# Performance work log

Hardware: AMD Instinct MI355X
Metric: run time of the kernel (lower is better)

## Reference

```python
import jax, jax.numpy as jnp
import numpy as np

N_EXPERTS = 16
TOP_K = 2
D_MODEL = 1024
D_FF = 1024
D_FF_SHARED = 2048
T_TOKENS = 4096


def setup_inputs() -> dict:
    key = jax.random.key(0)
    ks = jax.random.split(key, 7)
    s = 0.02
    return {
        "hidden_states": jax.random.normal(ks[0], (T_TOKENS, D_MODEL), jnp.float32),
        "gate_weight": jax.random.normal(ks[1], (N_EXPERTS, D_MODEL), jnp.float32) * s,
        "expert_gate_up": jax.random.normal(ks[2], (N_EXPERTS, 2 * D_FF, D_MODEL), jnp.float32) * s,
        "expert_down": jax.random.normal(ks[3], (N_EXPERTS, D_MODEL, D_FF), jnp.float32) * s,
        "shared_gate_up": jax.random.normal(ks[4], (2 * D_FF_SHARED, D_MODEL), jnp.float32) * s,
        "shared_down": jax.random.normal(ks[5], (D_MODEL, D_FF_SHARED), jnp.float32) * s,
        "shared_expert_gate_weight": jax.random.normal(ks[6], (1, D_MODEL), jnp.float32) * s,
    }


def _moe_forward(x, gate_weight, expert_gate_up, expert_down):
    T = x.shape[0]
    E = gate_weight.shape[0]
    # Router: top-k over logits, softmax over the selected logits (fp32)
    router_logits = x @ gate_weight.T                      # [T, E]
    topk_logits, topk_ids = jax.lax.top_k(router_logits, TOP_K)
    topk_weights = jax.nn.softmax(topk_logits.astype(jnp.float32), axis=-1)
    # Dense combine matrix C[t, e] = routing weight of expert e for token t
    combine = jnp.zeros((T, E), jnp.float32).at[
        jnp.arange(T)[:, None], topk_ids
    ].add(topk_weights)                                    # [T, E]

    # Scan over experts to avoid materializing [E, T, d]
    def body(acc, inputs):
        w_gu, w_d, c_e = inputs                            # [2F,d], [d,F], [T]
        gu = x @ w_gu.T                                    # [T, 2F]
        g, u = gu[:, :D_FF], gu[:, D_FF:]
        h = jax.nn.silu(g) * u                             # [T, F]
        acc = acc + c_e[:, None] * (h @ w_d.T)             # [T, d]
        return acc, None

    acc0 = jnp.zeros_like(x)
    moe_out, _ = jax.lax.scan(body, acc0, (expert_gate_up, expert_down, combine.T))
    return moe_out


def _shared_expert(x, shared_gate_up, shared_down, shared_expert_gate_weight):
    gu = x @ shared_gate_up.T                              # [T, 2Fs]
    mid = gu.shape[-1] // 2
    h = jax.nn.silu(gu[:, :mid]) * gu[:, mid:]
    out = h @ shared_down.T                                # [T, d]
    gate = jax.nn.sigmoid(x @ shared_expert_gate_weight.T)  # [T, 1]
    return out * gate


def reference(hidden_states, gate_weight, expert_gate_up, expert_down,
              shared_gate_up, shared_down, shared_expert_gate_weight):
    moe_out = _moe_forward(hidden_states, gate_weight, expert_gate_up, expert_down)
    shared_out = _shared_expert(hidden_states, shared_gate_up, shared_down,
                                shared_expert_gate_weight)
    return moe_out + shared_out
```

## Files before the change

kernel.cpp:

```cpp
#include <hip/hip_runtime.h>
#include <hip/hip_bf16.h>

#define T_TOKENS 4096
#define D_MODEL  1024
#define N_EXP    16
#define D_FF     1024
#define D_FF_SH  2048
#define MAX_T256 48

typedef __attribute__((ext_vector_type(8))) short short8;
typedef __attribute__((ext_vector_type(4))) float float4v;

__device__ __forceinline__ short f2bf(float f) {
    union { float f; unsigned u; } c; c.f = f;
    unsigned u = c.u + 0x7fffu + ((c.u >> 16) & 1u);
    return (short)(u >> 16);
}

__device__ __forceinline__ void gload16(const void* g, void* l) {
    __builtin_amdgcn_global_load_lds(
        (const __attribute__((address_space(1))) void*)g,
        (__attribute__((address_space(3))) void*)l, 16, 0, 0);
}

#define RING_TOP(VM) do { \
    asm volatile("s_waitcnt vmcnt(" #VM ") lgkmcnt(0)" ::: "memory"); \
    __builtin_amdgcn_s_barrier(); \
} while (0)

#define PHASE_BAR() do { \
    asm volatile("s_barrier" ::: "memory"); \
    __builtin_amdgcn_sched_barrier(0); \
} while (0)

__global__ __launch_bounds__(256) void convert_all_kernel(
    const float* __restrict__ s0, short* __restrict__ d0,
    const float* __restrict__ s1, short* __restrict__ d1,
    const float* __restrict__ s2, short* __restrict__ d2,
    const float* __restrict__ s3, short* __restrict__ d3) {
    int c = blockIdx.x * 256 + threadIdx.x;
    const float* s; short* d; int off;
    if      (c < 4194304) { s = s0; d = d0; off = c; }
    else if (c < 6291456) { s = s1; d = d1; off = c - 4194304; }
    else if (c < 6815744) { s = s2; d = d2; off = c - 6291456; }
    else                  { s = s3; d = d3; off = c - 6815744; }
    size_t i = (size_t)off * 8;
    float4 a = *(const float4*)(s + i);
    float4 b = *(const float4*)(s + i + 4);
    union { short sh[8]; int4 v; } p;
    p.sh[0] = f2bf(a.x); p.sh[1] = f2bf(a.y); p.sh[2] = f2bf(a.z); p.sh[3] = f2bf(a.w);
    p.sh[4] = f2bf(b.x); p.sh[5] = f2bf(b.y); p.sh[6] = f2bf(b.z); p.sh[7] = f2bf(b.w);
    *(int4*)(d + i) = p.v;
}

__global__ __launch_bounds__(256) void router_kernel(
    const float* __restrict__ x, const float* __restrict__ gw, const float* __restrict__ sgw,
    short* __restrict__ xb, int* __restrict__ topk_id, float* __restrict__ topk_w,
    float* __restrict__ gate, int* __restrict__ counts) {
    __shared__ float gwl[17 * 1024];
    int tid = threadIdx.x;
#pragma unroll
    for (int i = 0; i < 16; i++)
        *(float4*)&gwl[tid * 4 + i * 1024] = *(const float4*)&gw[tid * 4 + i * 1024];
    *(float4*)&gwl[16384 + tid * 4] = *(const float4*)&sgw[tid * 4];
    __syncthreads();

    int wave = tid >> 6, lane = tid & 63;
    int t0 = blockIdx.x * 16 + wave * 4;

    float acc[4][17];
#pragma unroll
    for (int tt = 0; tt < 4; tt++)
#pragma unroll
        for (int e = 0; e < 17; e++) acc[tt][e] = 0.f;

#pragma unroll
    for (int i = 0; i < 4; i++) {
        int d = lane * 4 + i * 256;
        float4 xv[4];
#pragma unroll
        for (int tt = 0; tt < 4; tt++) {
            xv[tt] = *(const float4*)&x[(size_t)(t0 + tt) * D_MODEL + d];
            union { short sh[4]; int2 v; } p;
            p.sh[0] = f2bf(xv[tt].x); p.sh[1] = f2bf(xv[tt].y);
            p.sh[2] = f2bf(xv[tt].z); p.sh[3] = f2bf(xv[tt].w);
            *(int2*)&xb[(size_t)(t0 + tt) * D_MODEL + d] = p.v;
        }
#pragma unroll
        for (int e = 0; e < 17; e++) {
            float4 g = *(const float4*)&gwl[e * 1024 + d];
#pragma unroll
            for (int tt = 0; tt < 4; tt++)
                acc[tt][e] += xv[tt].x * g.x + xv[tt].y * g.y + xv[tt].z * g.z + xv[tt].w * g.w;
        }
    }

#pragma unroll
    for (int tt = 0; tt < 4; tt++)
#pragma unroll
        for (int e = 0; e < 17; e++)
            for (int off = 32; off; off >>= 1) acc[tt][e] += __shfl_xor(acc[tt][e], off);

    if (lane == 0) {
#pragma unroll
        for (int tt = 0; tt < 4; tt++) {
            int t = t0 + tt;
            float v1 = -1e30f, v2 = -1e30f; int i1 = 0, i2 = 0;
#pragma unroll
            for (int e = 0; e < 16; e++) {
                float v = acc[tt][e];
                if (v > v1) { v2 = v1; i2 = i1; v1 = v; i1 = e; }
                else if (v > v2) { v2 = v; i2 = e; }
            }
            float e2 = expf(v2 - v1);
            float s = 1.f + e2;
            topk_id[t * 2] = i1; topk_id[t * 2 + 1] = i2;
            topk_w[t * 2] = 1.f / s; topk_w[t * 2 + 1] = e2 / s;
            gate[t] = 1.f / (1.f + expf(-acc[tt][16]));
            atomicAdd(&counts[i1], 1); atomicAdd(&counts[i2], 1);
        }
    }
}

__global__ void offsets_kernel(const int* __restrict__ counts, int* __restrict__ offsets,
                               int* __restrict__ cursor, int* __restrict__ tile_map,
                               int* __restrict__ n_tiles) {
    if (threadIdx.x == 0) {
        int off = 0, nt = 0;
        for (int e = 0; e < N_EXP; e++) {
            offsets[e] = off; cursor[e] = off;
            int c = counts[e];
            for (int r = 0; r < c; r += 256) tile_map[nt++] = (e << 16) | (r >> 8);
            off += c;
        }
        n_tiles[0] = nt;
    }
}

__global__ __launch_bounds__(256) void scatter_kernel(
    const int* __restrict__ topk_id, const float* __restrict__ topk_w,
    int* __restrict__ cursor, int* __restrict__ tok_list, float* __restrict__ tok_w,
    int* __restrict__ slot_of) {
    int t = blockIdx.x * 256 + threadIdx.x;
#pragma unroll
    for (int k = 0; k < 2; k++) {
        int e = topk_id[t * 2 + k];
        int pos = atomicAdd(&cursor[e], 1);
        tok_list[pos] = t;
        tok_w[pos] = topk_w[t * 2 + k];
        slot_of[t * 2 + k] = pos;
    }
}

__global__ __launch_bounds__(512, 2) void gemm1_kernel(
    const short* __restrict__ xb,
    const short* __restrict__ Wexp,
    const short* __restrict__ Wsh,
    short* __restrict__ Hexp,
    short* __restrict__ Hsh,
    const int* __restrict__ tok_list,
    const int* __restrict__ offsets, const int* __restrict__ counts,
    const int* __restrict__ tile_map, const int* __restrict__ n_tiles) {
    int bx = blockIdx.x, by = blockIdx.y;
    int count, row0, dff, col0;
    const int* idx = nullptr;
    const short* Wg; short* Hout;
    if (bx < MAX_T256) {
        if (bx >= n_tiles[0]) return;
        int tm = tile_map[bx];
        int e = tm >> 16; row0 = (tm & 0xffff) << 8;
        count = counts[e];
        int base = offsets[e];
        idx = tok_list + base;
        Wg = Wexp + (size_t)e * 2 * D_FF * D_MODEL;
        Hout = Hexp + (size_t)base * D_FF;
        dff = D_FF;
        col0 = by * 128;
    } else {
        int id = (bx - MAX_T256) * 8 + by;
        row0 = (id >> 4) * 256; count = T_TOKENS;
        Wg = Wsh; Hout = Hsh; dff = D_FF_SH;
        col0 = (id & 15) * 128;
    }
    const short* Wu = Wg + (size_t)dff * D_MODEL;

    __shared__ char lds[131072];

    int t = threadIdx.x;
    int wave = t >> 6, lane = t & 63;
    int wm = (wave & 3) * 64, wn = (wave >> 2) * 64;
    int fr = lane & 15;
    int fk2p = ((((lane >> 4) + (fr >> 1)) & 3) << 4);
    int rA = t >> 2;
    int csrc = ((t & 3) - (t >> 3)) & 3;
    int cq = csrc * 8;
    int lo = t * 16;

    int r0c = min(row0 + rA, count - 1);
    int r1c = min(row0 + rA + 128, count - 1);
    int g0 = idx ? idx[r0c] : r0c;
    int g1 = idx ? idx[r1c] : r1c;
    const short* aP0 = xb + (size_t)g0 * D_MODEL + cq;
    const short* aP1 = xb + (size_t)g1 * D_MODEL + cq;
    const short* bgP = Wg + (size_t)(col0 + rA) * D_MODEL + cq;
    const short* buP = Wu + (size_t)(col0 + rA) * D_MODEL + cq;

    float4v accg[4][4], accu[4][4];
#pragma unroll
    for (int i = 0; i < 4; i++)
#pragma unroll
        for (int j = 0; j < 4; j++) { accg[i][j] = (float4v)0.f; accu[i][j] = (float4v)0.f; }

    auto stage = [&](int s) {
        char* base = lds + (s & 3) * 32768;
        int off = s * 32;
        gload16(aP0 + off, base + lo);
        gload16(aP1 + off, base + 8192 + lo);
        gload16(bgP + off, base + 16384 + lo);
        gload16(buP + off, base + 24576 + lo);
    };

    auto step = [&](int k, bool pf) {
        const char* sb = lds + (k & 3) * 32768;
        char* nb = lds + ((k + 3) & 3) * 32768;
        int off3 = (k + 3) * 32;
        if (pf) { gload16(aP0 + off3, nb + lo); gload16(aP1 + off3, nb + 8192 + lo); }
        short8 af[4], bgf[4];
#pragma unroll
        for (int i = 0; i < 4; i++)
            af[i] = *(const short8*)(sb + (wm + i * 16 + fr) * 64 + fk2p);
#pragma unroll
        for (int j = 0; j < 4; j++)
            bgf[j] = *(const short8*)(sb + 16384 + (wn + j * 16 + fr) * 64 + fk2p);
        PHASE_BAR();
        __builtin_amdgcn_s_setprio(1);
#pragma unroll
        for (int i = 0; i < 4; i++)
#pragma unroll
            for (int j = 0; j < 4; j++)
                accg[i][j] = __builtin_amdgcn_mfma_f32_16x16x32_bf16(af[i], bgf[j], accg[i][j], 0, 0, 0);
        __builtin_amdgcn_s_setprio(0);
        if (pf) { gload16(bgP + off3, nb + 16384 + lo); gload16(buP + off3, nb + 24576 + lo); }
        short8 buf4[4];
#pragma unroll
        for (int j = 0; j < 4; j++)
            buf4[j] = *(const short8*)(sb + 24576 + (wn + j * 16 + fr) * 64 + fk2p);
        PHASE_BAR();
        __builtin_amdgcn_s_setprio(1);
#pragma unroll
        for (int i = 0; i < 4; i++)
#pragma unroll
            for (int j = 0; j < 4; j++)
                accu[i][j] = __builtin_amdgcn_mfma_f32_16x16x32_bf16(af[i], buf4[j], accu[i][j], 0, 0, 0);
        __builtin_amdgcn_s_setprio(0);
    };

    const int NK = D_MODEL / 32;
    stage(0); stage(1); stage(2);
    int k = 0;
    for (; k < NK - 3; ++k) { RING_TOP(8); step(k, true); }
    RING_TOP(8); step(k, false); ++k;
    RING_TOP(4); step(k, false); ++k;
    RING_TOP(0); step(k, false);

    int erow = (lane >> 4) * 4;
    int ecol = lane & 15;
#pragma unroll
    for (int i = 0; i < 4; i++)
#pragma unroll
        for (int j = 0; j < 4; j++)
#pragma unroll
            for (int r = 0; r < 4; r++) {
                int row = wm + i * 16 + erow + r;
                if (row0 + row < count) {
                    float g = accg[i][j][r], u = accu[i][j][r];
                    float h = g / (1.f + expf(-g)) * u;
                    Hout[(size_t)(row0 + row) * dff + col0 + wn + j * 16 + ecol] = f2bf(h);
                }
            }
}

__global__ __launch_bounds__(512, 4) void gemm2_kernel(
    const short* __restrict__ Hexp, const short* __restrict__ Hsh,
    const short* __restrict__ Wdexp,
    const short* __restrict__ Wdsh,
    float* __restrict__ oslots,
    float* __restrict__ out,
    const float* __restrict__ tok_w, const float* __restrict__ gate,
    const int* __restrict__ offsets, const int* __restrict__ counts,
    const int* __restrict__ tile_map, const int* __restrict__ n_tiles) {
    int bx = blockIdx.x, by = blockIdx.y;
    int count, row0, K, base, col0;
    const short* Ab; const short* B;
    bool shared_part;
    if (bx < 16) {
        int id = bx * 8 + by;
        row0 = (id >> 3) * 256; count = T_TOKENS; base = 0;
        Ab = Hsh; K = D_FF_SH; B = Wdsh; shared_part = true;
        col0 = (id & 7) * 128;
    } else {
        int q = bx - 16;
        if (q >= n_tiles[0]) return;
        int tm = tile_map[q];
        int e = tm >> 16; row0 = (tm & 0xffff) << 8;
        count = counts[e]; base = offsets[e];
        Ab = Hexp + (size_t)base * D_FF; K = D_FF;
        B = Wdexp + (size_t)e * D_MODEL * D_FF;
        shared_part = false;
        col0 = by * 128;
    }

    __shared__ char lds[73728];

    int t = threadIdx.x;
    int wave = t >> 6, lane = t & 63;
    int wm = (wave & 3) * 64, wn = (wave >> 2) * 64;
    int fr = lane & 15;
    int fk2p = ((((lane >> 4) + (fr >> 1)) & 3) << 4);
    int rA = t >> 2;
    int csrc = ((t & 3) - (t >> 3)) & 3;
    int cq = csrc * 8;
    int lo = t * 16;

    int r0c = min(row0 + rA, count - 1);
    int r1c = min(row0 + rA + 128, count - 1);
    const short* aP0 = Ab + (size_t)r0c * K + cq;
    const short* aP1 = Ab + (size_t)r1c * K + cq;
    const short* bP  = B + (size_t)(col0 + rA) * K + cq;

    float4v acc[4][4];
#pragma unroll
    for (int i = 0; i < 4; i++)
#pragma unroll
        for (int j = 0; j < 4; j++) acc[i][j] = (float4v)0.f;

    auto stage = [&](int pos, int s) {
        char* bb = lds + pos * 24576;
        int off = s * 32;
        gload16(aP0 + off, bb + lo);
        gload16(aP1 + off, bb + 8192 + lo);
        gload16(bP + off,  bb + 16384 + lo);
    };
    auto compute = [&](int pos) {
        const char* sb = lds + pos * 24576;
        short8 af[4], bf[4];
#pragma unroll
        for (int i = 0; i < 4; i++)
            af[i] = *(const short8*)(sb + (wm + i * 16 + fr) * 64 + fk2p);
#pragma unroll
        for (int j = 0; j < 4; j++)
            bf[j] = *(const short8*)(sb + 16384 + (wn + j * 16 + fr) * 64 + fk2p);
        __builtin_amdgcn_s_setprio(1);
#pragma unroll
        for (int i = 0; i < 4; i++)
#pragma unroll
            for (int j = 0; j < 4; j++)
                acc[i][j] = __builtin_amdgcn_mfma_f32_16x16x32_bf16(af[i], bf[j], acc[i][j], 0, 0, 0);
        __builtin_amdgcn_s_setprio(0);
    };

    const int NK = K / 32;
    stage(0, 0); stage(1, 1);
    int k = 0, spos = 2, cpos = 0;
    for (; k < NK - 2; ++k) {
        RING_TOP(3);
        stage(spos, k + 2); spos = (spos == 2) ? 0 : spos + 1;
        compute(cpos);      cpos = (cpos == 2) ? 0 : cpos + 1;
    }
    RING_TOP(3); compute(cpos); cpos = (cpos == 2) ? 0 : cpos + 1; ++k;
    RING_TOP(0); compute(cpos);

    int erow = (lane >> 4) * 4;
    int ecol = lane & 15;
#pragma unroll
    for (int i = 0; i < 4; i++)
#pragma unroll
        for (int j = 0; j < 4; j++)
#pragma unroll
            for (int r = 0; r < 4; r++) {
                int row = wm + i * 16 + erow + r;
                if (row0 + row < count) {
                    float v = acc[i][j][r];
                    int col = col0 + wn + j * 16 + ecol;
                    if (!shared_part) {
                        int slot = base + row0 + row;
                        oslots[(size_t)slot * D_MODEL + col] = tok_w[slot] * v;
                    } else {
                        out[(size_t)(row0 + row) * D_MODEL + col] = gate[row0 + row] * v;
                    }
                }
            }
}

__global__ __launch_bounds__(256) void combine_kernel(
    float* __restrict__ out, const float* __restrict__ oslots,
    const int* __restrict__ slot_of) {
    int t = blockIdx.x;
    int sA = slot_of[t * 2], sB = slot_of[t * 2 + 1];
    int d = threadIdx.x * 4;
    float4 o = *(float4*)&out[(size_t)t * D_MODEL + d];
    float4 a = *(const float4*)&oslots[(size_t)sA * D_MODEL + d];
    float4 b = *(const float4*)&oslots[(size_t)sB * D_MODEL + d];
    o.x += a.x + b.x; o.y += a.y + b.y; o.z += a.z + b.z; o.w += a.w + b.w;
    *(float4*)&out[(size_t)t * D_MODEL + d] = o;
}

extern "C" void kernel_launch(void* const* d_in, const int* in_sizes, int n_in,
                              void* d_out, int out_size, void* d_ws, size_t ws_size,
                              hipStream_t stream) {
    const float* x     = (const float*)d_in[0];
    const float* gw    = (const float*)d_in[1];
    const float* egu   = (const float*)d_in[2];
    const float* edown = (const float*)d_in[3];
    const float* sgu   = (const float*)d_in[4];
    const float* sdown = (const float*)d_in[5];
    const float* sgate = (const float*)d_in[6];
    float* out = (float*)d_out;
    char* ws = (char*)d_ws;

    const size_t XB_OFF     = 0;
    const size_t WGU_OFF    = XB_OFF     + (size_t)4096*1024*2;
    const size_t WDOWN_OFF  = WGU_OFF    + (size_t)16*2048*1024*2;
    const size_t WSGU_OFF   = WDOWN_OFF  + (size_t)16*1024*1024*2;
    const size_t WSDOWN_OFF = WSGU_OFF   + (size_t)4096*1024*2;
    const size_t HEXP_OFF   = WSDOWN_OFF + (size_t)1024*2048*2;
    const size_t HSH_OFF    = HEXP_OFF   + (size_t)8192*1024*2;
    const size_t OSLOT_OFF  = HSH_OFF    + (size_t)4096*2048*2;
    const size_t TID_OFF    = OSLOT_OFF  + (size_t)8192*1024*4;
    const size_t TW_OFF     = TID_OFF    + 4096*2*4;
    const size_t GATE_OFF   = TW_OFF     + 4096*2*4;
    const size_t TOKL_OFF   = GATE_OFF   + 4096*4;
    const size_t TOKW_OFF   = TOKL_OFF   + 8192*4;
    const size_t SLOT_OFF   = TOKW_OFF   + 8192*4;
    const size_t CNT_OFF    = SLOT_OFF   + 8192*4;
    const size_t OFFS_OFF   = CNT_OFF    + 256;
    const size_t CUR_OFF    = OFFS_OFF   + 256;
    const size_t TMAP_OFF   = CUR_OFF    + 256;
    const size_t NT_OFF     = TMAP_OFF   + 512;

    short* xb      = (short*)(ws + XB_OFF);
    short* wgu_b   = (short*)(ws + WGU_OFF);
    short* wdown_b = (short*)(ws + WDOWN_OFF);
    short* wsgu_b  = (short*)(ws + WSGU_OFF);
    short* wsdn_b  = (short*)(ws + WSDOWN_OFF);
    short* h_exp   = (short*)(ws + HEXP_OFF);
    short* h_sh    = (short*)(ws + HSH_OFF);
    float* oslots  = (float*)(ws + OSLOT_OFF);
    int*   topk_id = (int*)(ws + TID_OFF);
    float* topk_w  = (float*)(ws + TW_OFF);
    float* gate    = (float*)(ws + GATE_OFF);
    int*   tok_l   = (int*)(ws + TOKL_OFF);
    float* tok_w   = (float*)(ws + TOKW_OFF);
    int*   slot_of = (int*)(ws + SLOT_OFF);
    int*   counts  = (int*)(ws + CNT_OFF);
    int*   offsets = (int*)(ws + OFFS_OFF);
    int*   cursor  = (int*)(ws + CUR_OFF);
    int*   tmap    = (int*)(ws + TMAP_OFF);
    int*   ntiles  = (int*)(ws + NT_OFF);

    hipMemsetAsync(counts, 0, 64, stream);

    convert_all_kernel<<<27648, 256, 0, stream>>>(egu, wgu_b, edown, wdown_b,
                                                  sgu, wsgu_b, sdown, wsdn_b);
    router_kernel<<<256, 256, 0, stream>>>(x, gw, sgate, xb, topk_id, topk_w, gate, counts);
    offsets_kernel<<<1, 64, 0, stream>>>(counts, offsets, cursor, tmap, ntiles);
    scatter_kernel<<<T_TOKENS / 256, 256, 0, stream>>>(topk_id, topk_w, cursor, tok_l, tok_w, slot_of);

    gemm1_kernel<<<dim3(MAX_T256 + 32, 8), 512, 0, stream>>>(
        xb, wgu_b, wsgu_b, h_exp, h_sh, tok_l, offsets, counts, tmap, ntiles);

    gemm2_kernel<<<dim3(64, 8), 512, 0, stream>>>(
        h_exp, h_sh, wdown_b, wsdn_b, oslots, out, tok_w, gate, offsets, counts, tmap, ntiles);

    combine_kernel<<<T_TOKENS, 256, 0, stream>>>(out, oslots, slot_of);
}
```

Baseline: 593.0 us.

## Software-pipeline LDS fragment reads across k-steps in gate/up GEMM

```diff
diff --git a/kernel.cpp b/kernel.cpp
--- a/kernel.cpp
+++ b/kernel.cpp
@@ -26,11 +26,6 @@
 #define RING_TOP(VM) do { \
     asm volatile("s_waitcnt vmcnt(" #VM ") lgkmcnt(0)" ::: "memory"); \
     __builtin_amdgcn_s_barrier(); \
-} while (0)
-
-#define PHASE_BAR() do { \
-    asm volatile("s_barrier" ::: "memory"); \
-    __builtin_amdgcn_sched_barrier(0); \
 } while (0)
 
 __global__ __launch_bounds__(256) void convert_all_kernel(
@@ -220,48 +215,63 @@
         gload16(buP + off, base + 24576 + lo);
     };
 
-    auto step = [&](int k, bool pf) {
-        const char* sb = lds + (k & 3) * 32768;
-        char* nb = lds + ((k + 3) & 3) * 32768;
-        int off3 = (k + 3) * 32;
-        if (pf) { gload16(aP0 + off3, nb + lo); gload16(aP1 + off3, nb + 8192 + lo); }
-        short8 af[4], bgf[4];
-#pragma unroll
-        for (int i = 0; i < 4; i++)
-            af[i] = *(const short8*)(sb + (wm + i * 16 + fr) * 64 + fk2p);
-#pragma unroll
-        for (int j = 0; j < 4; j++)
-            bgf[j] = *(const short8*)(sb + 16384 + (wn + j * 16 + fr) * 64 + fk2p);
-        PHASE_BAR();
-        __builtin_amdgcn_s_setprio(1);
-#pragma unroll
-        for (int i = 0; i < 4; i++)
-#pragma unroll
-            for (int j = 0; j < 4; j++)
-                accg[i][j] = __builtin_amdgcn_mfma_f32_16x16x32_bf16(af[i], bgf[j], accg[i][j], 0, 0, 0);
-        __builtin_amdgcn_s_setprio(0);
-        if (pf) { gload16(bgP + off3, nb + 16384 + lo); gload16(buP + off3, nb + 24576 + lo); }
-        short8 buf4[4];
-#pragma unroll
-        for (int j = 0; j < 4; j++)
-            buf4[j] = *(const short8*)(sb + 24576 + (wn + j * 16 + fr) * 64 + fk2p);
-        PHASE_BAR();
-        __builtin_amdgcn_s_setprio(1);
-#pragma unroll
-        for (int i = 0; i < 4; i++)
-#pragma unroll
-            for (int j = 0; j < 4; j++)
-                accu[i][j] = __builtin_amdgcn_mfma_f32_16x16x32_bf16(af[i], buf4[j], accu[i][j], 0, 0, 0);
-        __builtin_amdgcn_s_setprio(0);
-    };
-
-    const int NK = D_MODEL / 32;
+    short8 afA[4], bgfA[4], bufA[4];
+    short8 afB[4], bgfB[4], bufB[4];
+
+#define G1_STEP(kk, DOSTAGE, WAITSTR, DOREAD, afC, bgfC, bufC, afN, bgfN) do { \
+    const char* sb_ = lds + ((kk) & 3) * 32768; \
+    if (DOSTAGE) stage((kk) + 3); \
+    _Pragma("unroll") \
+    for (int j_ = 0; j_ < 4; j_++) \
+        bufC[j_] = *(const short8*)(sb_ + 24576 + (wn + j_ * 16 + fr) * 64 + fk2p); \
+    __builtin_amdgcn_s_setprio(1); \
+    _Pragma("unroll") \
+    for (int i_ = 0; i_ < 4; i_++) \
+        _Pragma("unroll") \
+        for (int j_ = 0; j_ < 4; j_++) \
+            accg[i_][j_] = __builtin_amdgcn_mfma_f32_16x16x32_bf16(afC[i_], bgfC[j_], accg[i_][j_], 0, 0, 0); \
+    __builtin_amdgcn_s_setprio(0); \
+    asm volatile("s_waitcnt " WAITSTR ::: "memory"); \
+    asm volatile("s_barrier" ::: "memory"); \
+    __builtin_amdgcn_sched_barrier(0); \
+    if (DOREAD) { \
+        const char* nb_ = lds + (((kk) + 1) & 3) * 32768; \
+        _Pragma("unroll") \
+        for (int i_ = 0; i_ < 4; i_++) \
+            afN[i_] = *(const short8*)(nb_ + (wm + i_ * 16 + fr) * 64 + fk2p); \
+        _Pragma("unroll") \
+        for (int j_ = 0; j_ < 4; j_++) \
+            bgfN[j_] = *(const short8*)(nb_ + 16384 + (wn + j_ * 16 + fr) * 64 + fk2p); \
+    } \
+    __builtin_amdgcn_s_setprio(1); \
+    _Pragma("unroll") \
+    for (int i_ = 0; i_ < 4; i_++) \
+        _Pragma("unroll") \
+        for (int j_ = 0; j_ < 4; j_++) \
+            accu[i_][j_] = __builtin_amdgcn_mfma_f32_16x16x32_bf16(afC[i_], bufC[j_], accu[i_][j_], 0, 0, 0); \
+    __builtin_amdgcn_s_setprio(0); \
+} while (0)
+
     stage(0); stage(1); stage(2);
-    int k = 0;
-    for (; k < NK - 3; ++k) { RING_TOP(8); step(k, true); }
-    RING_TOP(8); step(k, false); ++k;
-    RING_TOP(4); step(k, false); ++k;
-    RING_TOP(0); step(k, false);
+    asm volatile("s_waitcnt vmcnt(8)" ::: "memory");
+    asm volatile("s_barrier" ::: "memory");
+    __builtin_amdgcn_sched_barrier(0);
+#pragma unroll
+    for (int i = 0; i < 4; i++)
+        afA[i] = *(const short8*)(lds + (wm + i * 16 + fr) * 64 + fk2p);
+#pragma unroll
+    for (int j = 0; j < 4; j++)
+        bgfA[j] = *(const short8*)(lds + 16384 + (wn + j * 16 + fr) * 64 + fk2p);
+
+    for (int k = 0; k < 28; k += 2) {
+        G1_STEP(k,     true, "vmcnt(8) lgkmcnt(0)", true, afA, bgfA, bufA, afB, bgfB);
+        G1_STEP(k + 1, true, "vmcnt(8) lgkmcnt(0)", true, afB, bgfB, bufB, afA, bgfA);
+    }
+    G1_STEP(28, true,  "vmcnt(8) lgkmcnt(0)", true,  afA, bgfA, bufA, afB, bgfB);
+    G1_STEP(29, false, "vmcnt(4) lgkmcnt(0)", true,  afB, bgfB, bufB, afA, bgfA);
+    G1_STEP(30, false, "vmcnt(0) lgkmcnt(0)", true,  afA, bgfA, bufA, afB, bgfB);
+    G1_STEP(31, false, "lgkmcnt(0)",          false, afB, bgfB, bufB, afA, bgfA);
+#undef G1_STEP
 
     int erow = (lane >> 4) * 4;
     int ecol = lane & 15;
```

Result: no change. 589.3 us (-0.6%).

## Fuse gate_up weight fp32-to-bf16 conversion into gemm1 through a register-staged pipeline

Applied to the files above, without the earlier changes.

```diff
diff --git a/kernel.cpp b/kernel.cpp
--- a/kernel.cpp
+++ b/kernel.cpp
@@ -28,22 +28,19 @@
     __builtin_amdgcn_s_barrier(); \
 } while (0)
 
-#define PHASE_BAR() do { \
-    asm volatile("s_barrier" ::: "memory"); \
+#define G1_TOP(WAITSTR) do { \
+    asm volatile("s_waitcnt " WAITSTR ::: "memory"); \
+    __builtin_amdgcn_s_barrier(); \
     __builtin_amdgcn_sched_barrier(0); \
 } while (0)
 
 __global__ __launch_bounds__(256) void convert_all_kernel(
-    const float* __restrict__ s0, short* __restrict__ d0,
     const float* __restrict__ s1, short* __restrict__ d1,
-    const float* __restrict__ s2, short* __restrict__ d2,
     const float* __restrict__ s3, short* __restrict__ d3) {
     int c = blockIdx.x * 256 + threadIdx.x;
     const float* s; short* d; int off;
-    if      (c < 4194304) { s = s0; d = d0; off = c; }
-    else if (c < 6291456) { s = s1; d = d1; off = c - 4194304; }
-    else if (c < 6815744) { s = s2; d = d2; off = c - 6291456; }
-    else                  { s = s3; d = d3; off = c - 6815744; }
+    if (c < 2097152) { s = s1; d = d1; off = c; }
+    else             { s = s3; d = d3; off = c - 2097152; }
     size_t i = (size_t)off * 8;
     float4 a = *(const float4*)(s + i);
     float4 b = *(const float4*)(s + i + 4);
@@ -154,8 +151,8 @@
 
 __global__ __launch_bounds__(512, 2) void gemm1_kernel(
     const short* __restrict__ xb,
-    const short* __restrict__ Wexp,
-    const short* __restrict__ Wsh,
+    const float* __restrict__ Wexp,
+    const float* __restrict__ Wsh,
     short* __restrict__ Hexp,
     short* __restrict__ Hsh,
     const int* __restrict__ tok_list,
@@ -164,7 +161,7 @@
     int bx = blockIdx.x, by = blockIdx.y;
     int count, row0, dff, col0;
     const int* idx = nullptr;
-    const short* Wg; short* Hout;
+    const float* Wg; short* Hout;
     if (bx < MAX_T256) {
         if (bx >= n_tiles[0]) return;
         int tm = tile_map[bx];
@@ -182,7 +179,7 @@
         Wg = Wsh; Hout = Hsh; dff = D_FF_SH;
         col0 = (id & 15) * 128;
     }
-    const short* Wu = Wg + (size_t)dff * D_MODEL;
+    const float* Wu = Wg + (size_t)dff * D_MODEL;
 
     __shared__ char lds[131072];
 
@@ -202,8 +199,8 @@
     int g1 = idx ? idx[r1c] : r1c;
     const short* aP0 = xb + (size_t)g0 * D_MODEL + cq;
     const short* aP1 = xb + (size_t)g1 * D_MODEL + cq;
-    const short* bgP = Wg + (size_t)(col0 + rA) * D_MODEL + cq;
-    const short* buP = Wu + (size_t)(col0 + rA) * D_MODEL + cq;
+    const float* bgP = Wg + (size_t)(col0 + rA) * D_MODEL + cq;
+    const float* buP = Wu + (size_t)(col0 + rA) * D_MODEL + cq;
 
     float4v accg[4][4], accu[4][4];
 #pragma unroll
@@ -211,57 +208,81 @@
 #pragma unroll
         for (int j = 0; j < 4; j++) { accg[i][j] = (float4v)0.f; accu[i][j] = (float4v)0.f; }
 
-    auto stage = [&](int s) {
+    float4 wg0, wg1, wu0, wu1;
+
+    auto astage = [&](int s) {
         char* base = lds + (s & 3) * 32768;
         int off = s * 32;
         gload16(aP0 + off, base + lo);
         gload16(aP1 + off, base + 8192 + lo);
-        gload16(bgP + off, base + 16384 + lo);
-        gload16(buP + off, base + 24576 + lo);
-    };
-
-    auto step = [&](int k, bool pf) {
+    };
+    auto wload = [&](int s) {
+        int off = s * 32;
+        wg0 = *(const float4*)(bgP + off);
+        wg1 = *(const float4*)(bgP + off + 4);
+        wu0 = *(const float4*)(buP + off);
+        wu1 = *(const float4*)(buP + off + 4);
+    };
+    auto wwrite = [&](int s) {
+        char* base = lds + (s & 3) * 32768;
+        union { short sh[8]; int4 v; } pg, pu;
+        pg.sh[0] = f2bf(wg0.x); pg.sh[1] = f2bf(wg0.y); pg.sh[2] = f2bf(wg0.z); pg.sh[3] = f2bf(wg0.w);
+        pg.sh[4] = f2bf(wg1.x); pg.sh[5] = f2bf(wg1.y); pg.sh[6] = f2bf(wg1.z); pg.sh[7] = f2bf(wg1.w);
+        pu.sh[0] = f2bf(wu0.x); pu.sh[1] = f2bf(wu0.y); pu.sh[2] = f2bf(wu0.z); pu.sh[3] = f2bf(wu0.w);
+        pu.sh[4] = f2bf(wu1.x); pu.sh[5] = f2bf(wu1.y); pu.sh[6] = f2bf(wu1.z); pu.sh[7] = f2bf(wu1.w);
+        *(int4*)(base + 16384 + lo) = pg.v;
+        *(int4*)(base + 24576 + lo) = pu.v;
+    };
+    auto compute = [&](int k) {
         const char* sb = lds + (k & 3) * 32768;
-        char* nb = lds + ((k + 3) & 3) * 32768;
-        int off3 = (k + 3) * 32;
-        if (pf) { gload16(aP0 + off3, nb + lo); gload16(aP1 + off3, nb + 8192 + lo); }
-        short8 af[4], bgf[4];
+        short8 af[4], bgf[4], buf4[4];
 #pragma unroll
         for (int i = 0; i < 4; i++)
             af[i] = *(const short8*)(sb + (wm + i * 16 + fr) * 64 + fk2p);
 #pragma unroll
-        for (int j = 0; j < 4; j++)
+        for (int j = 0; j < 4; j++) {
             bgf[j] = *(const short8*)(sb + 16384 + (wn + j * 16 + fr) * 64 + fk2p);
-        PHASE_BAR();
+            buf4[j] = *(const short8*)(sb + 24576 + (wn + j * 16 + fr) * 64 + fk2p);
+        }
         __builtin_amdgcn_s_setprio(1);
 #pragma unroll
         for (int i = 0; i < 4; i++)
 #pragma unroll
-            for (int j = 0; j < 4; j++)
+            for (int j = 0; j < 4; j++) {
                 accg[i][j] = __builtin_amdgcn_mfma_f32_16x16x32_bf16(af[i], bgf[j], accg[i][j], 0, 0, 0);
+                accu[i][j] = __builtin_amdgcn_mfma_f32_16x16x32_bf16(af[i], buf4[j], accu[i][j], 0, 0, 0);
+            }
         __builtin_amdgcn_s_setprio(0);
-        if (pf) { gload16(bgP + off3, nb + 16384 + lo); gload16(buP + off3, nb + 24576 + lo); }
-        short8 buf4[4];
-#pragma unroll
-        for (int j = 0; j < 4; j++)
-            buf4[j] = *(const short8*)(sb + 24576 + (wn + j * 16 + fr) * 64 + fk2p);
-        PHASE_BAR();
-        __builtin_amdgcn_s_setprio(1);
-#pragma unroll
-        for (int i = 0; i < 4; i++)
-#pragma unroll
-            for (int j = 0; j < 4; j++)
-                accu[i][j] = __builtin_amdgcn_mfma_f32_16x16x32_bf16(af[i], buf4[j], accu[i][j], 0, 0, 0);
-        __builtin_amdgcn_s_setprio(0);
-    };
-
-    const int NK = D_MODEL / 32;
-    stage(0); stage(1); stage(2);
-    int k = 0;
-    for (; k < NK - 3; ++k) { RING_TOP(8); step(k, true); }
-    RING_TOP(8); step(k, false); ++k;
-    RING_TOP(4); step(k, false); ++k;
-    RING_TOP(0); step(k, false);
+    };
+
+    wload(0);
+    asm volatile("" ::: "memory");
+    astage(0); astage(1); astage(2);
+    asm volatile("s_waitcnt vmcnt(6)" ::: "memory");
+    wwrite(0);
+    wload(1);
+
+    G1_TOP("vmcnt(0) lgkmcnt(0)");
+    wwrite(1); wload(2);
+    asm volatile("" ::: "memory");
+    astage(3);
+    compute(0);
+
+    for (int k = 1; k <= 28; ++k) {
+        G1_TOP("vmcnt(2) lgkmcnt(0)");
+        wwrite(k + 1); wload(k + 2);
+        asm volatile("" ::: "memory");
+        astage(k + 3);
+        compute(k);
+    }
+    G1_TOP("vmcnt(2) lgkmcnt(0)");
+    wwrite(30); wload(31);
+    compute(29);
+    G1_TOP("vmcnt(0) lgkmcnt(0)");
+    wwrite(31);
+    compute(30);
+    G1_TOP("lgkmcnt(0)");
+    compute(31);
 
     int erow = (lane >> 4) * 4;
     int ecol = lane & 15;
@@ -439,9 +460,7 @@
     const size_t NT_OFF     = TMAP_OFF   + 512;
 
     short* xb      = (short*)(ws + XB_OFF);
-    short* wgu_b   = (short*)(ws + WGU_OFF);
     short* wdown_b = (short*)(ws + WDOWN_OFF);
-    short* wsgu_b  = (short*)(ws + WSGU_OFF);
     short* wsdn_b  = (short*)(ws + WSDOWN_OFF);
     short* h_exp   = (short*)(ws + HEXP_OFF);
     short* h_sh    = (short*)(ws + HSH_OFF);
@@ -460,14 +479,13 @@
 
     hipMemsetAsync(counts, 0, 64, stream);
 
-    convert_all_kernel<<<27648, 256, 0, stream>>>(egu, wgu_b, edown, wdown_b,
-                                                  sgu, wsgu_b, sdown, wsdn_b);
+    convert_all_kernel<<<9216, 256, 0, stream>>>(edown, wdown_b, sdown, wsdn_b);
     router_kernel<<<256, 256, 0, stream>>>(x, gw, sgate, xb, topk_id, topk_w, gate, counts);
     offsets_kernel<<<1, 64, 0, stream>>>(counts, offsets, cursor, tmap, ntiles);
     scatter_kernel<<<T_TOKENS / 256, 256, 0, stream>>>(topk_id, topk_w, cursor, tok_l, tok_w, slot_of);
 
     gemm1_kernel<<<dim3(MAX_T256 + 32, 8), 512, 0, stream>>>(
-        xb, wgu_b, wsgu_b, h_exp, h_sh, tok_l, offsets, counts, tmap, ntiles);
+        xb, egu, sgu, h_exp, h_sh, tok_l, offsets, counts, tmap, ntiles);
 
     gemm2_kernel<<<dim3(64, 8), 512, 0, stream>>>(
         h_exp, h_sh, wdown_b, wsdn_b, oslots, out, tok_w, gate, offsets, counts, tmap, ntiles);
```

After: 601.7 us. About the same (+1.5%).
